# Kernel tuning notes

Measured on AMD Instinct MI355X. Metric: run time of the kernel, lower is better.

The kernel has to match this reference:

```python
import jax, jax.numpy as jnp
import numpy as np

B, N_SPINS, D_MODEL, K_MC = 256, 128, 768, 25


def setup_inputs() -> dict:
    key = jax.random.key(0)
    k1, k2, k3 = jax.random.split(key, 3)
    features = jax.random.normal(k1, (B, N_SPINS, D_MODEL), dtype=jnp.float32)
    coalitions = jax.random.randint(k2, (K_MC, N_SPINS), 0, 2, dtype=jnp.int32)
    w_v = jax.random.normal(k3, (D_MODEL, D_MODEL), dtype=jnp.float32) * 0.02
    scale = jnp.full((1,), 0.1, dtype=jnp.float32)
    return {"features": features, "coalitions": coalitions, "w_v": w_v, "scale": scale}


def reference(features, coalitions, w_v, scale):
    # features: [B, n, d]; coalitions: [K, n] in {0,1}; w_v: [d, d]; scale: [1]
    c = coalitions.astype(features.dtype)                      # [K, n]
    # coalition_value batched over all K coalitions at once:
    # sum_j mask[k,j] * features[b,j,:]  (sum and linear proj commute)
    s = jnp.einsum('kn,bnd->bkd', c, features)                 # [B, K, d]
    proj = s @ w_v                                             # [B, K, d]
    norm = jnp.linalg.norm(proj, axis=-1)                      # [B, K]
    cv = jax.nn.relu(norm * scale[0])                          # coalition values [B, K]
    # Shapley estimate: mean(v | i in S) - mean(v | i not in S)
    cnt_with = c.sum(axis=0)                                   # [n]
    cnt_without = c.shape[0] - cnt_with
    v_with = (cv @ c) / jnp.maximum(cnt_with, 1.0)             # [B, n]
    v_without = (cv @ (1.0 - c)) / jnp.maximum(cnt_without, 1.0)
    valid = (cnt_with > 0) & (cnt_without > 0)                 # [n]
    shapley = jnp.where(valid, v_with - v_without, 0.0)        # [B, n]
    return shapley
```

## Files before the change

### kernel.cpp

```cpp
#include <hip/hip_runtime.h>
#include <hip/hip_bf16.h>
#include <stdint.h>

#define NB  256
#define NSP 128
#define DM  768
#define KMC 25
#define MROWS (NB*KMC)

#define OFF_S    0u
#define OFF_WT   9830400u
#define OFF_N2   11010048u
#define OFF_COEF 11035648u

typedef __attribute__((ext_vector_type(8))) short bf16x8;
typedef __attribute__((ext_vector_type(4))) float f32x4;
typedef __attribute__((ext_vector_type(16))) float f32x16;
typedef unsigned int u32;

#define GLOAD_LDS16(gp, lp) \
  __builtin_amdgcn_global_load_lds((const __attribute__((address_space(1))) u32*)(gp), \
                                   (__attribute__((address_space(3))) u32*)(lp), 16, 0, 0)

#define KA_WAITV_BAR(N) asm volatile("s_waitcnt vmcnt(" #N ")\n\ts_barrier" ::: "memory")
#define KA_BAR()        asm volatile("s_barrier" ::: "memory")

#define KACH (16 * 384)

__global__ __launch_bounds__(256, 2) void kA_prep(const float* __restrict__ f,
                                                  const int* __restrict__ co,
                                                  const float* __restrict__ wv,
                                                  char* __restrict__ ws) {
  __shared__ __align__(16) char smem[3 * KACH * 4];
  const int bid = blockIdx.x;
  const int tid = threadIdx.x;

  if (bid >= 512) {
    const int blk = bid - 512;
    const int t = tid;
    if (blk < 144) {
      __hip_bfloat16 (*lt)[66] = (__hip_bfloat16(*)[66])smem;
      const int bi = blk / 12, bj = blk % 12;
      const int k0 = bi * 64, n0 = bj * 64;
      #pragma unroll
      for (int i = 0; i < 16; ++i) {
        int idx = t + i * 256;
        int r = idx >> 6, c = idx & 63;
        lt[c][r] = __float2bfloat16(wv[(size_t)(k0 + r) * DM + n0 + c]);
      }
      __syncthreads();
      __hip_bfloat16* wT = (__hip_bfloat16*)(ws + OFF_WT);
      #pragma unroll
      for (int i = 0; i < 16; ++i) {
        int idx = t + i * 256;
        int r = idx >> 6, c = idx & 63;
        wT[(size_t)(n0 + r) * DM + k0 + c] = lt[r][c];
      }
    } else if (blk == 144) {
      if (t < NSP) {
        const int n = t;
        int cw = 0;
        #pragma unroll
        for (int k = 0; k < KMC; ++k) cw += co[k * NSP + n];
        const int cwo = KMC - cw;
        const bool valid = (cw > 0) && (cwo > 0);
        float* coefT = (float*)(ws + OFF_COEF);
        #pragma unroll
        for (int k = 0; k < 28; ++k) {
          float v = 0.f;
          if (valid && k < KMC) v = co[k * NSP + n] ? (1.f / (float)cw) : (-1.f / (float)cwo);
          coefT[n * 28 + k] = v;
        }
      }
    } else {
      int i = (blk - 145) * 256 + t;
      if (i < MROWS) ((float*)(ws + OFF_N2))[i] = 0.f;
    }
    return;
  }

  const int b = bid >> 1;
  const int half = bid & 1;
  const int w = tid >> 6;
  const int lane = tid & 63;
  const int l31 = lane & 31, l5 = lane >> 5;

  float (*Fs)[KACH] = (float(*)[KACH])smem;
  __hip_bfloat16* s = (__hip_bfloat16*)(ws + OFF_S);

  bf16x8 Af[8];
  #pragma unroll
  for (int ks = 0; ks < 8; ++ks) {
    if (l31 < KMC) {
      const int* cp = co + l31 * NSP + ks * 16 + l5 * 8;
      int4 c0 = *(const int4*)(cp);
      int4 c1 = *(const int4*)(cp + 4);
      __hip_bfloat16 h;
      h = __float2bfloat16((float)c0.x); Af[ks][0] = *(short*)&h;
      h = __float2bfloat16((float)c0.y); Af[ks][1] = *(short*)&h;
      h = __float2bfloat16((float)c0.z); Af[ks][2] = *(short*)&h;
      h = __float2bfloat16((float)c0.w); Af[ks][3] = *(short*)&h;
      h = __float2bfloat16((float)c1.x); Af[ks][4] = *(short*)&h;
      h = __float2bfloat16((float)c1.y); Af[ks][5] = *(short*)&h;
      h = __float2bfloat16((float)c1.z); Af[ks][6] = *(short*)&h;
      h = __float2bfloat16((float)c1.w); Af[ks][7] = *(short*)&h;
    } else {
      #pragma unroll
      for (int j = 0; j < 8; ++j) Af[ks][j] = 0;
    }
  }
  asm volatile("s_waitcnt vmcnt(0)" ::: "memory");

  const float* fb = f + (size_t)b * NSP * DM + half * 384;
  int goff[6];
  #pragma unroll
  for (int q = 0; q < 6; ++q) {
    int e = (w * 6 + q) * 256 + lane * 4;
    int r = e / 384, c = e - r * 384;
    goff[q] = r * DM + c;
  }

  f32x16 ac[3];
  #pragma unroll
  for (int nt = 0; nt < 3; ++nt)
    #pragma unroll
    for (int r = 0; r < 16; ++r) ac[nt][r] = 0.f;

#define KA_ISSUE(ck, bi) { \
    const float* fp_ = fb + (size_t)(ck) * 16 * DM; \
    _Pragma("unroll") for (int q = 0; q < 6; ++q) \
      GLOAD_LDS16(fp_ + goff[q], (char*)&Fs[(bi)][0] + ((w * 6 + q) << 10)); }

#define KA_MFMA(ks, bi) { \
    _Pragma("unroll") for (int nt = 0; nt < 3; ++nt) { \
      bf16x8 Bf; \
      _Pragma("unroll") for (int j = 0; j < 8; ++j) { \
        float v_ = Fs[(bi)][(l5 * 8 + j) * 384 + w * 96 + nt * 32 + l31]; \
        __hip_bfloat16 h_ = __float2bfloat16(v_); \
        Bf[j] = *(short*)&h_; } \
      ac[nt] = __builtin_amdgcn_mfma_f32_32x32x16_bf16(Af[ks], Bf, ac[nt], 0, 0, 0); } }

  KA_ISSUE(0, 0) KA_ISSUE(1, 1) KA_ISSUE(2, 2)
  KA_WAITV_BAR(12);  KA_MFMA(0, 0)  KA_BAR();  KA_ISSUE(3, 0)
  KA_WAITV_BAR(12);  KA_MFMA(1, 1)  KA_BAR();  KA_ISSUE(4, 1)
  KA_WAITV_BAR(12);  KA_MFMA(2, 2)  KA_BAR();  KA_ISSUE(5, 2)
  KA_WAITV_BAR(12);  KA_MFMA(3, 0)  KA_BAR();  KA_ISSUE(6, 0)
  KA_WAITV_BAR(12);  KA_MFMA(4, 1)  KA_BAR();  KA_ISSUE(7, 1)
  KA_WAITV_BAR(12);  KA_MFMA(5, 2)
  KA_WAITV_BAR(6);   KA_MFMA(6, 0)
  KA_WAITV_BAR(0);   KA_MFMA(7, 1)

#undef KA_ISSUE
#undef KA_MFMA

  #pragma unroll
  for (int nt = 0; nt < 3; ++nt) {
    int dcol = half * 384 + w * 96 + nt * 32 + l31;
    #pragma unroll
    for (int r = 0; r < 16; ++r) {
      int row = (r & 3) + 8 * (r >> 2) + 4 * l5;
      if (row < KMC)
        s[((size_t)b * KMC + row) * DM + dcol] = __float2bfloat16(ac[nt][r]);
    }
  }
}

#define BM 64
#define BN 192
#define BK 32
#define NTK 24

__global__ __launch_bounds__(256) void kB(char* __restrict__ ws) {
  const int hwbid = blockIdx.x;
  const int bid = (hwbid & 7) * 50 + (hwbid >> 3);
  const int tm = bid >> 2;
  const int tn = bid & 3;
  const int tid = threadIdx.x;
  const int wid = tid >> 6;
  const int lane = tid & 63;
  const int wm = wid >> 1;
  const int wn = wid & 1;

  const __hip_bfloat16* S  = (const __hip_bfloat16*)(ws + OFF_S);
  const __hip_bfloat16* WT = (const __hip_bfloat16*)(ws + OFF_WT);
  float* norm2 = (float*)(ws + OFF_N2);

  __shared__ __align__(16) char As[2][BM * BK * 2];
  __shared__ __align__(16) char Bs[2][BN * BK * 2];

  const char* gA; char *lAA0, *lAA1;
  {
    int li = wid * 64 + lane;
    int r = li >> 2, sl = li & 3;
    int slx = sl ^ ((r >> 1) & 3);
    gA = (const char*)(S + (size_t)(tm * BM + r) * DM) + slx * 16;
    lAA0 = As[0] + wid * 1024;
    lAA1 = As[1] + wid * 1024;
  }
  const char* gB[3]; char *lB0[3], *lB1[3];
  #pragma unroll
  for (int j = 0; j < 3; ++j) {
    int li = (wid * 3 + j) * 64 + lane;
    int r = li >> 2, sl = li & 3;
    int slx = sl ^ ((r >> 1) & 3);
    gB[j] = (const char*)(WT + (size_t)(tn * BN + r) * DM) + slx * 16;
    lB0[j] = Bs[0] + (wid * 3 + j) * 1024;
    lB1[j] = Bs[1] + (wid * 3 + j) * 1024;
  }

  auto stage = [&](int tk, int bsel) {
    size_t koff = (size_t)tk * (BK * 2);
    GLOAD_LDS16(gA + koff, bsel ? lAA1 : lAA0);
    #pragma unroll
    for (int j = 0; j < 3; ++j) GLOAD_LDS16(gB[j] + koff, bsel ? lB1[j] : lB0[j]);
  };

  f32x4 acc[2][6];
  #pragma unroll
  for (int m = 0; m < 2; ++m)
    #pragma unroll
    for (int n = 0; n < 6; ++n)
      #pragma unroll
      for (int j = 0; j < 4; ++j) acc[m][n][j] = 0.f;

  int offA[2], offB[6];
  #pragma unroll
  for (int m = 0; m < 2; ++m) {
    int r = wm * 32 + m * 16 + (lane & 15);
    int sl = (lane >> 4) ^ ((r >> 1) & 3);
    offA[m] = r * 64 + sl * 16;
  }
  #pragma unroll
  for (int n = 0; n < 6; ++n) {
    int r = wn * 96 + n * 16 + (lane & 15);
    int sl = (lane >> 4) ^ ((r >> 1) & 3);
    offB[n] = r * 64 + sl * 16;
  }

  stage(0, 0);
  for (int tk = 0; tk < NTK; ++tk) {
    int cur = tk & 1;
    __syncthreads();
    if (tk + 1 < NTK) stage(tk + 1, cur ^ 1);
    bf16x8 af[2], bfr[6];
    #pragma unroll
    for (int m = 0; m < 2; ++m) af[m] = *(const bf16x8*)(As[cur] + offA[m]);
    #pragma unroll
    for (int n = 0; n < 6; ++n) bfr[n] = *(const bf16x8*)(Bs[cur] + offB[n]);
    #pragma unroll
    for (int m = 0; m < 2; ++m)
      #pragma unroll
      for (int n = 0; n < 6; ++n)
        acc[m][n] = __builtin_amdgcn_mfma_f32_16x16x32_bf16(af[m], bfr[n], acc[m][n], 0, 0, 0);
  }

  float ps[2][4];
  #pragma unroll
  for (int m = 0; m < 2; ++m)
    #pragma unroll
    for (int i = 0; i < 4; ++i) {
      float v = 0.f;
      #pragma unroll
      for (int n = 0; n < 6; ++n) { float x = acc[m][n][i]; v += x * x; }
      #pragma unroll
      for (int d = 1; d < 16; d <<= 1) v += __shfl_xor(v, d, 64);
      ps[m][i] = v;
    }
  if ((lane & 15) == 0) {
    int g = lane >> 4;
    #pragma unroll
    for (int m = 0; m < 2; ++m)
      #pragma unroll
      for (int i = 0; i < 4; ++i)
        atomicAdd(&norm2[tm * BM + wm * 32 + m * 16 + g * 4 + i], ps[m][i]);
  }
}

__global__ __launch_bounds__(128) void kC(const char* __restrict__ ws,
                                          const float* __restrict__ scale,
                                          float* __restrict__ out) {
  const int b = blockIdx.x, n = threadIdx.x;
  const float* norm2 = (const float*)(ws + OFF_N2);
  const float* coefT = (const float*)(ws + OFF_COEF);
  __shared__ float cvs[32];
  if (n < KMC) {
    float nv = norm2[b * KMC + n];
    cvs[n] = fmaxf(sqrtf(fmaxf(nv, 0.f)) * scale[0], 0.f);
  } else if (n < 32) {
    cvs[n] = 0.f;
  }
  __syncthreads();
  float sum = 0.f;
  #pragma unroll
  for (int k = 0; k < KMC; ++k) sum += cvs[k] * coefT[n * 28 + k];
  out[b * NSP + n] = sum;
}

extern "C" void kernel_launch(void* const* d_in, const int* in_sizes, int n_in,
                              void* d_out, int out_size, void* d_ws, size_t ws_size,
                              hipStream_t stream) {
  const float* features   = (const float*)d_in[0];
  const int*   coalitions = (const int*)d_in[1];
  const float* wv         = (const float*)d_in[2];
  const float* scale      = (const float*)d_in[3];
  char* ws = (char*)d_ws;

  kA_prep<<<682, 256, 0, stream>>>(features, coalitions, wv, ws);
  kB<<<400, 256, 0, stream>>>(ws);
  kC<<<NB, 128, 0, stream>>>(ws, scale, (float*)d_out);
}
```

Baseline: 42.40 us.

## Prefetch two K-tiles ahead in GEMM with explicit vmcnt waits

Restructures the GEMM main loop to issue loads for two tiles before computing. It replaces __syncthreads with explicit s_waitcnt vmcnt/lgkmcnt plus barrier, so global-to-LDS loads for tile k+2 overlap MFMA on tile k. The loop is fully unrolled. It relies on hand-counted vmcnt values (4 outstanding) matching the number of loads per stage; a wrong count would cause races.

```diff
diff --git a/kernel.cpp b/kernel.cpp
--- a/kernel.cpp
+++ b/kernel.cpp
@@ -24,6 +24,7 @@
 
 #define KA_WAITV_BAR(N) asm volatile("s_waitcnt vmcnt(" #N ")\n\ts_barrier" ::: "memory")
 #define KA_BAR()        asm volatile("s_barrier" ::: "memory")
+#define KB_RETIRE_BAR() asm volatile("s_waitcnt lgkmcnt(0)\n\ts_barrier" ::: "memory")
 
 #define KACH (16 * 384)
 
@@ -237,22 +238,32 @@
     offB[n] = r * 64 + sl * 16;
   }
 
+#define KB_MFMA(cur) { \
+    bf16x8 af[2], bfr[6]; \
+    _Pragma("unroll") for (int m = 0; m < 2; ++m) \
+      af[m] = *(const bf16x8*)(As[cur] + offA[m]); \
+    _Pragma("unroll") for (int n = 0; n < 6; ++n) \
+      bfr[n] = *(const bf16x8*)(Bs[cur] + offB[n]); \
+    _Pragma("unroll") for (int m = 0; m < 2; ++m) \
+      _Pragma("unroll") for (int n = 0; n < 6; ++n) \
+        acc[m][n] = __builtin_amdgcn_mfma_f32_16x16x32_bf16(af[m], bfr[n], acc[m][n], 0, 0, 0); }
+
+  asm volatile("s_waitcnt vmcnt(0)" ::: "memory");
   stage(0, 0);
-  for (int tk = 0; tk < NTK; ++tk) {
-    int cur = tk & 1;
-    __syncthreads();
-    if (tk + 1 < NTK) stage(tk + 1, cur ^ 1);
-    bf16x8 af[2], bfr[6];
-    #pragma unroll
-    for (int m = 0; m < 2; ++m) af[m] = *(const bf16x8*)(As[cur] + offA[m]);
-    #pragma unroll
-    for (int n = 0; n < 6; ++n) bfr[n] = *(const bf16x8*)(Bs[cur] + offB[n]);
-    #pragma unroll
-    for (int m = 0; m < 2; ++m)
-      #pragma unroll
-      for (int n = 0; n < 6; ++n)
-        acc[m][n] = __builtin_amdgcn_mfma_f32_16x16x32_bf16(af[m], bfr[n], acc[m][n], 0, 0, 0);
-  }
+  stage(1, 1);
+  #pragma unroll
+  for (int tk = 0; tk < NTK - 1; ++tk) {
+    KA_WAITV_BAR(4);
+    KB_MFMA(tk & 1)
+    if (tk + 2 < NTK) {
+      KB_RETIRE_BAR();
+      stage(tk + 2, tk & 1);
+    }
+  }
+  KA_WAITV_BAR(0);
+  KB_MFMA((NTK - 1) & 1)
+
+#undef KB_MFMA
 
   float ps[2][4];
   #pragma unroll
```

New measurement: 42.45 us. Within noise of the previous version (+0.1%).
